# Optimization experiments

Hardware: AMD Instinct MI355X
Metric: run time of the kernel (lower is better)

Reference implementation:

```python
import jax, jax.numpy as jnp
import numpy as np

B, N = 64, 512          # batch (Multiple*BatchSize), nodes per graph
LIT, SEM = 128, 64      # literal / semantic feature widths
ED, HD, OD = 64, 32, 64 # EmbedDim, HalfDim (hardcoded 32), OutputDim
ITERS, ELAYERS = 5, 2   # IteraTimes, EmbedLayer


def setup_inputs() -> dict:
    key = jax.random.key(0)
    ks = jax.random.split(key, 32)
    s = 0.05
    inp = {
        "cfg1": jax.random.randint(ks[0], (B, N, N), 0, 2, dtype=jnp.int32),
        "pfg1": jax.random.randint(ks[1], (B, N, N), 0, 2, dtype=jnp.int32),
        "lit1": jax.random.normal(ks[2], (B, N, LIT), dtype=jnp.float32),
        "sem1": jax.random.normal(ks[3], (B, N, SEM), dtype=jnp.float32),
        "cfg2": jax.random.randint(ks[4], (B, N, N), 0, 2, dtype=jnp.int32),
        "pfg2": jax.random.randint(ks[5], (B, N, N), 0, 2, dtype=jnp.int32),
        "lit2": jax.random.normal(ks[6], (B, N, LIT), dtype=jnp.float32),
        "sem2": jax.random.normal(ks[7], (B, N, SEM), dtype=jnp.float32),
    }
    # branch 1 (MyDataLayer #1) params
    inp["d1w1"] = jax.random.normal(ks[8], (LIT, ED)) * s
    inp["d1b1"] = jnp.zeros((ED,), jnp.float32)
    inp["d2w1"] = jax.random.normal(ks[9], (ED, HD)) * s
    inp["d2b1"] = jnp.zeros((HD,), jnp.float32)
    inp["lk1"] = jax.random.normal(ks[10], (SEM, 4 * HD)) * s
    inp["lrk1"] = jax.random.normal(ks[11], (HD, 4 * HD)) * s
    inp["lb1"] = jnp.zeros((4 * HD,), jnp.float32)
    # branch 2 (MyDataLayer #2) params
    inp["d1w2"] = jax.random.normal(ks[12], (LIT, ED)) * s
    inp["d1b2"] = jnp.zeros((ED,), jnp.float32)
    inp["d2w2"] = jax.random.normal(ks[13], (ED, HD)) * s
    inp["d2b2"] = jnp.zeros((HD,), jnp.float32)
    inp["lk2"] = jax.random.normal(ks[14], (SEM, 4 * HD)) * s
    inp["lrk2"] = jax.random.normal(ks[15], (HD, 4 * HD)) * s
    inp["lb2"] = jnp.zeros((4 * HD,), jnp.float32)
    # shared MyEmbedLayer params
    inp["we_w"] = jax.random.normal(ks[16], (ELAYERS, ED, ED)) * s
    inp["we_b"] = jnp.zeros((ELAYERS, ED), jnp.float32)
    inp["wout"] = jax.random.normal(ks[17], (ED, OD)) * s
    inp["bout"] = jnp.zeros((OD,), jnp.float32)
    return inp


def _lstm(x, k, rk, b):
    # x: [B, T, D]; Keras gate order i, f, c(g), o; sigmoid recurrent activation
    h0 = jnp.zeros((x.shape[0], rk.shape[0]), x.dtype)

    def step(carry, xt):
        h, c = carry
        z = xt @ k + h @ rk + b
        i, f, g, o = jnp.split(z, 4, axis=-1)
        c = jax.nn.sigmoid(f) * c + jax.nn.sigmoid(i) * jnp.tanh(g)
        h = jax.nn.sigmoid(o) * jnp.tanh(c)
        return (h, c), h

    _, hs = jax.lax.scan(step, (h0, h0), jnp.swapaxes(x, 0, 1))
    return jnp.swapaxes(hs, 0, 1)  # [B, T, HD]


def _branch(lit, sem, d1w, d1b, d2w, d2b, lk, lrk, lb):
    mlp = jax.nn.relu(jax.nn.relu(lit @ d1w + d1b) @ d2w + d2b)  # [B,N,HD]
    return jnp.concatenate([mlp, _lstm(sem, lk, lrk, lb)], axis=-1)  # [B,N,ED]


def _embed(inp, adj, we_w, we_b, wout, bout):
    x = jax.nn.relu(inp)
    for _ in range(ITERS):
        t = adj @ x  # [B,N,N] @ [B,N,ED] -> message passing
        for l in range(ELAYERS):
            t = jax.nn.relu(t @ we_w[l] + we_b[l])
        x = jnp.tanh(inp + t)
    return x.sum(axis=1) @ wout + bout  # [B, OD]


def reference(cfg1, pfg1, lit1, sem1, cfg2, pfg2, lit2, sem2,
              d1w1, d1b1, d2w1, d2b1, lk1, lrk1, lb1,
              d1w2, d1b2, d2w2, d2b2, lk2, lrk2, lb2,
              we_w, we_b, wout, bout):
    bb1 = _branch(lit1, sem1, d1w1, d1b1, d2w1, d2b1, lk1, lrk1, lb1)
    e1 = _embed(bb1, cfg1.astype(jnp.float32), we_w, we_b, wout, bout)
    bb2 = _branch(lit2, sem2, d1w2, d1b2, d2w2, d2b2, lk2, lrk2, lb2)
    e2 = _embed(bb2, cfg2.astype(jnp.float32), we_w, we_b, wout, bout)
    num = jnp.sum(e1 * e2, axis=1)
    den = jnp.sqrt(jnp.sum(e1 ** 2, axis=1) * jnp.sum(e2 ** 2, axis=1) + 1e-10)
    return num / den  # [B]
```

## Files before the change

kernel.cpp:

```cpp
#include <hip/hip_runtime.h>

#define DEV static __device__ __forceinline__

typedef float  f32x2 __attribute__((ext_vector_type(2)));
typedef float  f32x4 __attribute__((ext_vector_type(4)));
typedef float  f32x8 __attribute__((ext_vector_type(8)));
typedef __bf16 bf16x8 __attribute__((ext_vector_type(8)));
typedef unsigned short u16x8 __attribute__((ext_vector_type(8)));
typedef int    i32x4 __attribute__((ext_vector_type(4)));

DEV unsigned short f2bf(float f) {
  unsigned u = __builtin_bit_cast(unsigned, f);
  u += 0x7FFFu + ((u >> 16) & 1u);
  return (unsigned short)(u >> 16);
}
DEV float bf2f(unsigned short h) {
  unsigned u = (unsigned)h << 16;
  return __builtin_bit_cast(float, u);
}

DEV f32x4 mfma16(u16x8 a, u16x8 b, f32x4 c) {
  return __builtin_amdgcn_mfma_f32_16x16x32_bf16(
      __builtin_bit_cast(bf16x8, a), __builtin_bit_cast(bf16x8, b), c, 0, 0, 0);
}
DEV i32x4 mfma8(uint4 a, uint4 b, i32x4 c) {
  return __builtin_amdgcn_mfma_i32_16x16x64_i8(
      __builtin_bit_cast(i32x4, a), __builtin_bit_cast(i32x4, b), c, 0, 0, 0);
}

DEV float exp2_hw(float x) { float r; asm("v_exp_f32 %0, %1" : "=v"(r) : "v"(x)); return r; }
DEV float sig_fast(float x) { return __builtin_amdgcn_rcpf(1.f + exp2_hw(-1.44269504f * x)); }
DEV float tanh_fast(float x) { return 1.f - 2.f * __builtin_amdgcn_rcpf(exp2_hw(2.88539008f * x) + 1.f); }

DEV void pkfma(f32x2& acc, f32x2 a, f32x2 b) {
  asm("v_pk_fma_f32 %0, %1, %2, %0" : "+v"(acc) : "v"(a), "v"(b));
}

DEV uint4 expand16(unsigned hw) {
  uint4 r;
  r.x = ((hw         & 0xFu) * 0x00204081u) & 0x01010101u;
  r.y = (((hw >> 4)  & 0xFu) * 0x00204081u) & 0x01010101u;
  r.z = (((hw >> 8)  & 0xFu) * 0x00204081u) & 0x01010101u;
  r.w = (((hw >> 12) & 0xFu) * 0x00204081u) & 0x01010101u;
  return r;
}

DEV void split8(const float* p, u16x8& h, u16x8& l) {
  union { f32x4 q[2]; f32x8 o; } u;
  u.q[0] = *reinterpret_cast<const f32x4*>(p);
  u.q[1] = *reinterpret_cast<const f32x4*>(p + 4);
  #pragma unroll
  for (int i = 0; i < 8; ++i) {
    float v = u.o[i];
    unsigned short hb = f2bf(v);
    h[i] = hb;
    l[i] = f2bf(v - bf2f(hb));
  }
}

template <int K, int NC, int ACT>
__global__ __launch_bounds__(256) void k_ff(
    const float* __restrict__ A1, const float* __restrict__ A2,
    const float* __restrict__ W1, const float* __restrict__ W2,
    const float* __restrict__ b1, const float* __restrict__ b2,
    float* __restrict__ C, int ldC, long brCstride) {
  int bid = blockIdx.x;
  int br = bid >> 8, rbk = bid & 255;
  const float* A = br ? A2 : A1;
  const float* W = br ? W2 : W1;
  const float* bias = br ? b2 : b1;

  __shared__ __attribute__((aligned(16))) unsigned short WTh[NC][K + 8];
  __shared__ __attribute__((aligned(16))) unsigned short WTl[NC][K + 8];
  for (int idx = threadIdx.x; idx < K * NC; idx += 256) {
    int k = idx / NC, c = idx % NC;
    float w = W[idx];
    unsigned short hb = f2bf(w);
    WTh[c][k] = hb;
    WTl[c][k] = f2bf(w - bf2f(hb));
  }
  __syncthreads();

  int wave = threadIdx.x >> 6, lane = threadIdx.x & 63;
  int l15 = lane & 15, g = lane >> 4;
  int row0 = rbk * 128 + wave * 32;

  f32x4 acc[2][NC / 16] = {};
  for (int kk = 0; kk < K; kk += 32) {
    u16x8 ah[2], al[2];
    #pragma unroll
    for (int rt = 0; rt < 2; ++rt)
      split8(A + (size_t)(row0 + rt * 16 + l15) * K + kk + g * 8, ah[rt], al[rt]);
    #pragma unroll
    for (int ct = 0; ct < NC / 16; ++ct) {
      u16x8 wh = *reinterpret_cast<const u16x8*>(&WTh[ct * 16 + l15][kk + g * 8]);
      u16x8 wl = *reinterpret_cast<const u16x8*>(&WTl[ct * 16 + l15][kk + g * 8]);
      #pragma unroll
      for (int rt = 0; rt < 2; ++rt) {
        acc[rt][ct] = mfma16(ah[rt], wh, acc[rt][ct]);
        acc[rt][ct] = mfma16(al[rt], wh, acc[rt][ct]);
        acc[rt][ct] = mfma16(ah[rt], wl, acc[rt][ct]);
      }
    }
  }

  float bv[NC / 16];
  #pragma unroll
  for (int ct = 0; ct < NC / 16; ++ct) bv[ct] = bias[ct * 16 + l15];
  #pragma unroll
  for (int rt = 0; rt < 2; ++rt)
    #pragma unroll
    for (int ct = 0; ct < NC / 16; ++ct)
      #pragma unroll
      for (int r = 0; r < 4; ++r) {
        float v = acc[rt][ct][r] + bv[ct];
        if (ACT) v = fmaxf(v, 0.f);
        C[(size_t)br * brCstride +
          (size_t)(row0 + rt * 16 + g * 4 + r) * ldC + ct * 16 + l15] = v;
      }
}

__global__ __launch_bounds__(256) void k_front(
    const float* __restrict__ xk,
    const float* __restrict__ lrk1, const float* __restrict__ lrk2,
    float* __restrict__ bb,
    const int* __restrict__ cfg1, const int* __restrict__ cfg2,
    unsigned* __restrict__ bits,
    const float* __restrict__ lit1, const float* __restrict__ lit2,
    const float* __restrict__ d1w1, const float* __restrict__ d1w2,
    const float* __restrict__ d1b1, const float* __restrict__ d1b2,
    const float* __restrict__ d2w1, const float* __restrict__ d2w2,
    const float* __restrict__ d2b1, const float* __restrict__ d2b2) {
  __shared__ __attribute__((aligned(16))) unsigned short WT1h[64][136];
  __shared__ __attribute__((aligned(16))) unsigned short WT1l[64][136];
  __shared__ __attribute__((aligned(16))) unsigned short WT2h[32][72];
  __shared__ __attribute__((aligned(16))) unsigned short WT2l[32][72];
  __shared__ __attribute__((aligned(16))) float H1[128][68];
  __shared__ __attribute__((aligned(16))) float sh[4][64];
  __shared__ __attribute__((aligned(16))) float lds_pad[520];

  int bid = blockIdx.x;
  int wave = threadIdx.x >> 6, lane = threadIdx.x & 63;
  if (bid == 0x3FFFFFFF) ((volatile float*)lds_pad)[threadIdx.x & 511] = 1.f;

  if (bid < 32) {
    int gb = bid * 4 + wave;
    int br = gb >> 6, b = gb & 63;
    int u = lane & 31, hi = lane >> 5;
    int c0 = u + (hi << 5), c1 = c0 + 64;
    const float* rkp = br ? lrk2 : lrk1;
    f32x2 rk0p[16], rk1p[16];
    #pragma unroll
    for (int k2 = 0; k2 < 16; ++k2) {
      rk0p[k2] = f32x2{rkp[(2 * k2) * 128 + c0], rkp[(2 * k2 + 1) * 128 + c0]};
      rk1p[k2] = f32x2{rkp[(2 * k2) * 128 + c1], rkp[(2 * k2 + 1) * 128 + c1]};
    }
    float* shw = &sh[wave][0];
    shw[lane] = 0.f;

    const float* xkb = xk + ((size_t)br * 32768 + (size_t)b * 512) * 128;
    float* bbo = bb + ((size_t)br * 32768 + (size_t)b * 512) * 64 + 32;
    float cst = 0.f;

    float z00 = xkb[0 * 128 + c0], z10 = xkb[0 * 128 + c1];
    float z01 = xkb[1 * 128 + c0], z11 = xkb[1 * 128 + c1];
    float z02 = xkb[2 * 128 + c0], z12 = xkb[2 * 128 + c1];
    float z03 = xkb[3 * 128 + c0], z13 = xkb[3 * 128 + c1];
    float z04 = xkb[4 * 128 + c0], z14 = xkb[4 * 128 + c1];
    float z05 = xkb[5 * 128 + c0], z15 = xkb[5 * 128 + c1];
    float z06 = xkb[6 * 128 + c0], z16 = xkb[6 * 128 + c1];
    float z07 = xkb[7 * 128 + c0], z17 = xkb[7 * 128 + c1];

    union Q { f32x4 q; f32x2 p[2]; };

#define LSTM_STEP(T, ZA, ZB) {                                          \
    float a0 = ZA, a1 = ZB;                                             \
    ZA = xkb[((T) + 8) * 128 + c0]; ZB = xkb[((T) + 8) * 128 + c1];     \
    Q q0, q1, q2, q3, q4, q5, q6, q7;                                   \
    q0.q = *reinterpret_cast<const f32x4*>(&shw[32]);                   \
    q1.q = *reinterpret_cast<const f32x4*>(&shw[36]);                   \
    q2.q = *reinterpret_cast<const f32x4*>(&shw[40]);                   \
    q3.q = *reinterpret_cast<const f32x4*>(&shw[44]);                   \
    q4.q = *reinterpret_cast<const f32x4*>(&shw[48]);                   \
    q5.q = *reinterpret_cast<const f32x4*>(&shw[52]);                   \
    q6.q = *reinterpret_cast<const f32x4*>(&shw[56]);                   \
    q7.q = *reinterpret_cast<const f32x4*>(&shw[60]);                   \
    f32x2 A0 = {0.f, 0.f}, A1 = {0.f, 0.f};                             \
    f32x2 B0 = {0.f, 0.f}, B1 = {0.f, 0.f};                             \
    pkfma(A0, q0.p[0], rk0p[0]);  pkfma(B0, q0.p[0], rk1p[0]);          \
    pkfma(A1, q0.p[1], rk0p[1]);  pkfma(B1, q0.p[1], rk1p[1]);          \
    pkfma(A0, q1.p[0], rk0p[2]);  pkfma(B0, q1.p[0], rk1p[2]);          \
    pkfma(A1, q1.p[1], rk0p[3]);  pkfma(B1, q1.p[1], rk1p[3]);          \
    pkfma(A0, q2.p[0], rk0p[4]);  pkfma(B0, q2.p[0], rk1p[4]);          \
    pkfma(A1, q2.p[1], rk0p[5]);  pkfma(B1, q2.p[1], rk1p[5]);          \
    pkfma(A0, q3.p[0], rk0p[6]);  pkfma(B0, q3.p[0], rk1p[6]);          \
    pkfma(A1, q3.p[1], rk0p[7]);  pkfma(B1, q3.p[1], rk1p[7]);          \
    pkfma(A0, q4.p[0], rk0p[8]);  pkfma(B0, q4.p[0], rk1p[8]);          \
    pkfma(A1, q4.p[1], rk0p[9]);  pkfma(B1, q4.p[1], rk1p[9]);          \
    pkfma(A0, q5.p[0], rk0p[10]); pkfma(B0, q5.p[0], rk1p[10]);         \
    pkfma(A1, q5.p[1], rk0p[11]); pkfma(B1, q5.p[1], rk1p[11]);         \
    pkfma(A0, q6.p[0], rk0p[12]); pkfma(B0, q6.p[0], rk1p[12]);         \
    pkfma(A1, q6.p[1], rk0p[13]); pkfma(B1, q6.p[1], rk1p[13]);         \
    pkfma(A0, q7.p[0], rk0p[14]); pkfma(B0, q7.p[0], rk1p[14]);         \
    pkfma(A1, q7.p[1], rk0p[15]); pkfma(B1, q7.p[1], rk1p[15]);         \
    float a0f = a0 + (A0.x + A1.x) + (A0.y + A1.y);                     \
    float a1f = a1 + (B0.x + B1.x) + (B0.y + B1.y);                     \
    float s0 = sig_fast(a0f);                     \
    float s1 = hi ? sig_fast(a1f) : tanh_fast(a1f);  \
    float at = s0 * s1;                           \
    float rc = __shfl_xor(at, 32);                                      \
    cst = s0 * cst + rc;                          \
    float hv = s1 * tanh_fast(cst);                                     \
    shw[lane] = hv;                                                     \
    if (hi) bbo[(T) * 64 + u] = hv;                                     \
  }

    for (int tb = 0; tb < 512; tb += 8) {
      LSTM_STEP(tb + 0, z00, z10)
      LSTM_STEP(tb + 1, z01, z11)
      LSTM_STEP(tb + 2, z02, z12)
      LSTM_STEP(tb + 3, z03, z13)
      LSTM_STEP(tb + 4, z04, z14)
      LSTM_STEP(tb + 5, z05, z15)
      LSTM_STEP(tb + 6, z06, z16)
      LSTM_STEP(tb + 7, z07, z17)
    }
#undef LSTM_STEP
    return;
  }

  if (bid < 288) {
    unsigned worker = (unsigned)(bid - 32) * 256u + threadIdx.x;
    #pragma unroll
    for (int j = 0; j < 16; ++j) {
      unsigned idx = worker + (unsigned)j * 65536u;
      unsigned br2 = idx >> 19;
      unsigned rem = idx & 524287u;
      const int4* p = reinterpret_cast<const int4*>(br2 ? cfg2 : cfg1) + rem * 8;
      unsigned m = 0;
      #pragma unroll
      for (int q = 0; q < 8; ++q) {
        int4 v = p[q];
        unsigned base = q * 4;
        m |= ((unsigned)v.x & 1u) << (base + 0);
        m |= ((unsigned)v.y & 1u) << (base + 1);
        m |= ((unsigned)v.z & 1u) << (base + 2);
        m |= ((unsigned)v.w & 1u) << (base + 3);
      }
      bits[idx] = m;
    }
    return;
  }

  int bid2 = bid - 288;
  int br = bid2 >> 8, rbk = bid2 & 255;
  const float* lit = br ? lit2 : lit1;
  const float* W1  = br ? d1w2 : d1w1;
  const float* B1  = br ? d1b2 : d1b1;
  const float* W2  = br ? d2w2 : d2w1;
  const float* B2  = br ? d2b2 : d2b1;

  for (int idx = threadIdx.x; idx < 8192; idx += 256) {
    int k = idx >> 6, c = idx & 63;
    float w = W1[idx];
    unsigned short hb = f2bf(w);
    WT1h[c][k] = hb;
    WT1l[c][k] = f2bf(w - bf2f(hb));
  }
  for (int idx = threadIdx.x; idx < 2048; idx += 256) {
    int k = idx >> 5, c = idx & 31;
    float w = W2[idx];
    unsigned short hb = f2bf(w);
    WT2h[c][k] = hb;
    WT2l[c][k] = f2bf(w - bf2f(hb));
  }
  __syncthreads();

  int l15 = lane & 15, g = lane >> 4;
  int row0 = rbk * 128 + wave * 32;

  f32x4 acc[2][4] = {};
  #pragma unroll
  for (int kk = 0; kk < 128; kk += 32) {
    u16x8 ah[2], al[2];
    #pragma unroll
    for (int rt = 0; rt < 2; ++rt)
      split8(lit + (size_t)(row0 + rt * 16 + l15) * 128 + kk + g * 8, ah[rt], al[rt]);
    #pragma unroll
    for (int ct = 0; ct < 4; ++ct) {
      u16x8 wh = *reinterpret_cast<const u16x8*>(&WT1h[ct * 16 + l15][kk + g * 8]);
      u16x8 wl = *reinterpret_cast<const u16x8*>(&WT1l[ct * 16 + l15][kk + g * 8]);
      #pragma unroll
      for (int rt = 0; rt < 2; ++rt) {
        acc[rt][ct] = mfma16(ah[rt], wh, acc[rt][ct]);
        acc[rt][ct] = mfma16(al[rt], wh, acc[rt][ct]);
        acc[rt][ct] = mfma16(ah[rt], wl, acc[rt][ct]);
      }
    }
  }
  #pragma unroll
  for (int ct = 0; ct < 4; ++ct) {
    float bv = B1[ct * 16 + l15];
    #pragma unroll
    for (int rt = 0; rt < 2; ++rt)
      #pragma unroll
      for (int r = 0; r < 4; ++r)
        H1[wave * 32 + rt * 16 + g * 4 + r][ct * 16 + l15] =
            fmaxf(acc[rt][ct][r] + bv, 0.f);
  }
  f32x4 acc2[2][2] = {};
  #pragma unroll
  for (int kk = 0; kk < 64; kk += 32) {
    u16x8 ah[2], al[2];
    #pragma unroll
    for (int rt = 0; rt < 2; ++rt)
      split8(&H1[wave * 32 + rt * 16 + l15][kk + g * 8], ah[rt], al[rt]);
    #pragma unroll
    for (int ct = 0; ct < 2; ++ct) {
      u16x8 wh = *reinterpret_cast<const u16x8*>(&WT2h[ct * 16 + l15][kk + g * 8]);
      u16x8 wl = *reinterpret_cast<const u16x8*>(&WT2l[ct * 16 + l15][kk + g * 8]);
      #pragma unroll
      for (int rt = 0; rt < 2; ++rt) {
        acc2[rt][ct] = mfma16(ah[rt], wh, acc2[rt][ct]);
        acc2[rt][ct] = mfma16(al[rt], wh, acc2[rt][ct]);
        acc2[rt][ct] = mfma16(ah[rt], wl, acc2[rt][ct]);
      }
    }
  }
  #pragma unroll
  for (int ct = 0; ct < 2; ++ct) {
    float bv = B2[ct * 16 + l15];
    #pragma unroll
    for (int rt = 0; rt < 2; ++rt)
      #pragma unroll
      for (int r = 0; r < 4; ++r)
        bb[((size_t)br * 32768 + row0 + rt * 16 + g * 4 + r) * 64 + ct * 16 + l15] =
            fmaxf(acc2[rt][ct][r] + bv, 0.f);
  }
}

__global__ __launch_bounds__(256) void k_relu_t(const float* __restrict__ bb,
                                                unsigned short* __restrict__ XTh,
                                                unsigned short* __restrict__ XTl) {
  int bid = blockIdx.x;
  int br = bid >> 9, rem = bid & 511, b = rem >> 3, tile = rem & 7;
  int n0 = tile * 64;
  __shared__ unsigned short xh[64][65], xl[64][65];
  const f32x4* src =
      reinterpret_cast<const f32x4*>(bb + ((size_t)(br * 64 + b) * 512 + n0) * 64);
  #pragma unroll
  for (int i = 0; i < 4; ++i) {
    int f = i * 256 + threadIdx.x;
    f32x4 v = src[f];
    int n = f >> 4, c4 = (f & 15) * 4;
    #pragma unroll
    for (int j = 0; j < 4; ++j) {
      float val = fmaxf(v[j], 0.f);
      unsigned short hb = f2bf(val);
      xh[n][c4 + j] = hb;
      xl[n][c4 + j] = f2bf(val - bf2f(hb));
    }
  }
  __syncthreads();
  int c = threadIdx.x >> 2, j0 = (threadIdx.x & 3) * 16;
  size_t base = ((size_t)(br * 64 + b) * 64 + c) * 512 + n0 + j0;
  u16x8 o0, o1, p0, p1;
  #pragma unroll
  for (int i = 0; i < 8; ++i) {
    o0[i] = xh[j0 + i][c]; o1[i] = xh[j0 + 8 + i][c];
    p0[i] = xl[j0 + i][c]; p1[i] = xl[j0 + 8 + i][c];
  }
  *reinterpret_cast<u16x8*>(XTh + base) = o0;
  *reinterpret_cast<u16x8*>(XTh + base + 8) = o1;
  *reinterpret_cast<u16x8*>(XTl + base) = p0;
  *reinterpret_cast<u16x8*>(XTl + base + 8) = p1;
}

template <int AIN8, int LAST>
__global__ __launch_bounds__(256, 2) void k_iter(
    const unsigned* __restrict__ bits,
    const unsigned short* __restrict__ XTbfh, const unsigned short* __restrict__ XTbfl,
    const char* __restrict__ X8h_in, const char* __restrict__ X8l_in,
    const float* __restrict__ bb,
    const float* __restrict__ we_w, const float* __restrict__ we_b,
    char* __restrict__ X8h_out, char* __restrict__ X8l_out,
    float* __restrict__ Spart) {
  int bid = blockIdx.x;
  int rb = bid >> 7, br = (bid >> 6) & 1, b = bid & 63;
  int n0 = rb * 256;
  __shared__ __attribute__((aligned(16))) unsigned short WT0h[64][72];
  __shared__ __attribute__((aligned(16))) unsigned short WT0l[64][72];
  __shared__ __attribute__((aligned(16))) unsigned short WT1h[64][72];
  __shared__ __attribute__((aligned(16))) unsigned short WT1l[64][72];
  __shared__ __attribute__((aligned(16))) char uni[34816];
  __shared__ float colsum[16][64];
  auto ts  = reinterpret_cast<float(*)[32][68]>(uni);
  auto xh8 = reinterpret_cast<char(*)[65]>(uni);
  auto xl8 = reinterpret_cast<char(*)[65]>(uni + 8320);

  for (int idx = threadIdx.x; idx < 4096; idx += 256) {
    int k = idx >> 6, c = idx & 63;
    float w0 = we_w[k * 64 + c], w1 = we_w[4096 + k * 64 + c];
    unsigned short h0 = f2bf(w0), h1b = f2bf(w1);
    WT0h[c][k] = h0; WT0l[c][k] = f2bf(w0 - bf2f(h0));
    WT1h[c][k] = h1b; WT1l[c][k] = f2bf(w1 - bf2f(h1b));
  }
  __syncthreads();

  int wave = threadIdx.x >> 6, lane = threadIdx.x & 63;
  int l15 = lane & 15, g = lane >> 4;
  int rowbase = n0 + wave * 64;

  union BWU { uint4 v[4]; unsigned w[16]; };
  BWU bw0, bw1, bw2, bw3;
  {
    const unsigned* p0 =
        bits + (size_t)br * 524288 + ((size_t)b * 512 + rowbase + l15) * 16;
    #pragma unroll
    for (int q = 0; q < 4; ++q) {
      bw0.v[q] = reinterpret_cast<const uint4*>(p0)[q];
      bw1.v[q] = reinterpret_cast<const uint4*>(p0 + 256)[q];
      bw2.v[q] = reinterpret_cast<const uint4*>(p0 + 512)[q];
      bw3.v[q] = reinterpret_cast<const uint4*>(p0 + 768)[q];
    }
  }

  float tv[4][4][4];

  if constexpr (!AIN8) {
    size_t xtbase = (size_t)(br * 64 + b) * 64 * 512;
    f32x4 acc[4][4] = {};
    #pragma unroll
    for (int kk = 0; kk < 512; kk += 32) {
      u16x8 a0, a1, a2, a3;
      {
        unsigned w0 = bw0.w[kk >> 5] >> (g * 8), w1 = bw1.w[kk >> 5] >> (g * 8);
        unsigned w2 = bw2.w[kk >> 5] >> (g * 8), w3 = bw3.w[kk >> 5] >> (g * 8);
        union { unsigned u[4]; u16x8 v; } r0, r1, r2, r3;
        #pragma unroll
        for (int i = 0; i < 4; ++i) {
          r0.u[i] = (((w0 >> (2 * i)) & 1u) ? 0x3F80u : 0u) |
                    (((w0 >> (2 * i + 1)) & 1u) ? 0x3F800000u : 0u);
          r1.u[i] = (((w1 >> (2 * i)) & 1u) ? 0x3F80u : 0u) |
                    (((w1 >> (2 * i + 1)) & 1u) ? 0x3F800000u : 0u);
          r2.u[i] = (((w2 >> (2 * i)) & 1u) ? 0x3F80u : 0u) |
                    (((w2 >> (2 * i + 1)) & 1u) ? 0x3F800000u : 0u);
          r3.u[i] = (((w3 >> (2 * i)) & 1u) ? 0x3F80u : 0u) |
                    (((w3 >> (2 * i + 1)) & 1u) ? 0x3F800000u : 0u);
        }
        a0 = r0.v; a1 = r1.v; a2 = r2.v; a3 = r3.v;
      }
      #pragma unroll
      for (int ct = 0; ct < 4; ++ct) {
        size_t off = xtbase + (size_t)(ct * 16 + l15) * 512 + kk + g * 8;
        u16x8 bh = *reinterpret_cast<const u16x8*>(XTbfh + off);
        u16x8 bl = *reinterpret_cast<const u16x8*>(XTbfl + off);
        acc[0][ct] = mfma16(a0, bh, acc[0][ct]);
        acc[0][ct] = mfma16(a0, bl, acc[0][ct]);
        acc[1][ct] = mfma16(a1, bh, acc[1][ct]);
        acc[1][ct] = mfma16(a1, bl, acc[1][ct]);
        acc[2][ct] = mfma16(a2, bh, acc[2][ct]);
        acc[2][ct] = mfma16(a2, bl, acc[2][ct]);
        acc[3][ct] = mfma16(a3, bh, acc[3][ct]);
        acc[3][ct] = mfma16(a3, bl, acc[3][ct]);
      }
    }
    #pragma unroll
    for (int rt = 0; rt < 4; ++rt)
      #pragma unroll
      for (int ct = 0; ct < 4; ++ct)
        #pragma unroll
        for (int r = 0; r < 4; ++r)
          tv[rt][ct][r] = acc[rt][ct][r];
  } else {
    size_t x8base = (size_t)(br * 64 + b) * 64 * 512;
    i32x4 acch[4][4] = {};
    i32x4 accl[4][4] = {};
    #pragma unroll
    for (int c64 = 0; c64 < 8; ++c64) {
      int kk = c64 * 64;
      int wi = (kk >> 5) + (g >> 1), shv = (g & 1) * 16;
      uint4 a0 = expand16((bw0.w[wi] >> shv) & 0xFFFFu);
      uint4 a1 = expand16((bw1.w[wi] >> shv) & 0xFFFFu);
      uint4 a2 = expand16((bw2.w[wi] >> shv) & 0xFFFFu);
      uint4 a3 = expand16((bw3.w[wi] >> shv) & 0xFFFFu);
      #pragma unroll
      for (int ct = 0; ct < 4; ++ct) {
        size_t off = x8base + (size_t)(ct * 16 + l15) * 512 + kk + g * 16;
        uint4 bh = *reinterpret_cast<const uint4*>(X8h_in + off);
        uint4 bl = *reinterpret_cast<const uint4*>(X8l_in + off);
        acch[0][ct] = mfma8(a0, bh, acch[0][ct]);
        accl[0][ct] = mfma8(a0, bl, accl[0][ct]);
        acch[1][ct] = mfma8(a1, bh, acch[1][ct]);
        accl[1][ct] = mfma8(a1, bl, accl[1][ct]);
        acch[2][ct] = mfma8(a2, bh, acch[2][ct]);
        accl[2][ct] = mfma8(a2, bl, accl[2][ct]);
        acch[3][ct] = mfma8(a3, bh, acch[3][ct]);
        accl[3][ct] = mfma8(a3, bl, accl[3][ct]);
      }
    }
    #pragma unroll
    for (int rt = 0; rt < 4; ++rt)
      #pragma unroll
      for (int ct = 0; ct < 4; ++ct)
        #pragma unroll
        for (int r = 0; r < 4; ++r)
          tv[rt][ct][r] = (float)acch[rt][ct][r] * (1.f / 127.f) +
                          (float)accl[rt][ct][r] * (1.f / 16129.f);
  }

  float sacc[4] = {0.f, 0.f, 0.f, 0.f};

  #pragma unroll
  for (int p = 0; p < 2; ++p) {
    if (!LAST && p) __syncthreads();

    #pragma unroll
    for (int rt = 0; rt < 2; ++rt)
      #pragma unroll
      for (int ct = 0; ct < 4; ++ct)
        #pragma unroll
        for (int r = 0; r < 4; ++r)
          ts[wave][rt * 16 + g * 4 + r][ct * 16 + l15] = tv[2 * p + rt][ct][r];

    f32x4 acc1[2][4] = {};
    #pragma unroll
    for (int kk = 0; kk < 64; kk += 32) {
      u16x8 ah[2], al[2];
      #pragma unroll
      for (int rt = 0; rt < 2; ++rt)
        split8(&ts[wave][rt * 16 + l15][kk + g * 8], ah[rt], al[rt]);
      #pragma unroll
      for (int ct = 0; ct < 4; ++ct) {
        u16x8 wh = *reinterpret_cast<const u16x8*>(&WT0h[ct * 16 + l15][kk + g * 8]);
        u16x8 wl = *reinterpret_cast<const u16x8*>(&WT0l[ct * 16 + l15][kk + g * 8]);
        #pragma unroll
        for (int rt = 0; rt < 2; ++rt) {
          acc1[rt][ct] = mfma16(ah[rt], wh, acc1[rt][ct]);
          acc1[rt][ct] = mfma16(al[rt], wh, acc1[rt][ct]);
          acc1[rt][ct] = mfma16(ah[rt], wl, acc1[rt][ct]);
        }
      }
    }
    #pragma unroll
    for (int rt = 0; rt < 2; ++rt)
      #pragma unroll
      for (int ct = 0; ct < 4; ++ct) {
        float bv = we_b[ct * 16 + l15];
        #pragma unroll
        for (int r = 0; r < 4; ++r)
          ts[wave][rt * 16 + g * 4 + r][ct * 16 + l15] =
              fmaxf(acc1[rt][ct][r] + bv, 0.f);
      }

    f32x4 acc2[2][4] = {};
    #pragma unroll
    for (int kk = 0; kk < 64; kk += 32) {
      u16x8 ah[2], al[2];
      #pragma unroll
      for (int rt = 0; rt < 2; ++rt)
        split8(&ts[wave][rt * 16 + l15][kk + g * 8], ah[rt], al[rt]);
      #pragma unroll
      for (int ct = 0; ct < 4; ++ct) {
        u16x8 wh = *reinterpret_cast<const u16x8*>(&WT1h[ct * 16 + l15][kk + g * 8]);
        u16x8 wl = *reinterpret_cast<const u16x8*>(&WT1l[ct * 16 + l15][kk + g * 8]);
        #pragma unroll
        for (int rt = 0; rt < 2; ++rt) {
          acc2[rt][ct] = mfma16(ah[rt], wh, acc2[rt][ct]);
          acc2[rt][ct] = mfma16(al[rt], wh, acc2[rt][ct]);
          acc2[rt][ct] = mfma16(ah[rt], wl, acc2[rt][ct]);
        }
      }
    }

    const float* bbrow =
        bb + ((size_t)(br * 64 + b) * 512 + rowbase + p * 32) * 64;

    if (!LAST) {
      __syncthreads();
      #pragma unroll
      for (int rt = 0; rt < 2; ++rt)
        #pragma unroll
        for (int ct = 0; ct < 4; ++ct) {
          float bv = we_b[64 + ct * 16 + l15];
          #pragma unroll
          for (int r = 0; r < 4; ++r) {
            int rr = rt * 16 + g * 4 + r, cc = ct * 16 + l15;
            float t3 = fmaxf(acc2[rt][ct][r] + bv, 0.f);
            float v = tanh_fast(bbrow[rr * 64 + cc] + t3);
            float s = v * 127.f;
            float qhf = rintf(s);
            float qlf = rintf((s - qhf) * 127.f);
            xh8[wave * 32 + rr][cc] = (char)(int)qhf;
            xl8[wave * 32 + rr][cc] = (char)(int)qlf;
          }
        }
      __syncthreads();
      int c = threadIdx.x >> 2, w4 = threadIdx.x & 3;
      int j0 = w4 * 32;
      size_t base = ((size_t)(br * 64 + b) * 64 + c) * 512 + n0 + w4 * 64 + p * 32;
      union { uint4 v[2]; char bch[32]; } oh, ol;
      #pragma unroll
      for (int i = 0; i < 32; ++i) {
        oh.bch[i] = xh8[j0 + i][c];
        ol.bch[i] = xl8[j0 + i][c];
      }
      *reinterpret_cast<uint4*>(X8h_out + base) = oh.v[0];
      *reinterpret_cast<uint4*>(X8h_out + base + 16) = oh.v[1];
      *reinterpret_cast<uint4*>(X8l_out + base) = ol.v[0];
      *reinterpret_cast<uint4*>(X8l_out + base + 16) = ol.v[1];
    } else {
      #pragma unroll
      for (int ct = 0; ct < 4; ++ct) {
        float bv = we_b[64 + ct * 16 + l15];
        float s = 0.f;
        #pragma unroll
        for (int rt = 0; rt < 2; ++rt)
          #pragma unroll
          for (int r = 0; r < 4; ++r) {
            int rr = rt * 16 + g * 4 + r, cc = ct * 16 + l15;
            float t3 = fmaxf(acc2[rt][ct][r] + bv, 0.f);
            s += tanh_fast(bbrow[rr * 64 + cc] + t3);
          }
        sacc[ct] += s;
      }
    }
  }

  if (LAST) {
    #pragma unroll
    for (int ct = 0; ct < 4; ++ct)
      colsum[wave * 4 + g][ct * 16 + l15] = sacc[ct];
    __syncthreads();
    if (threadIdx.x < 64) {
      float s = 0.f;
      #pragma unroll
      for (int q = 0; q < 16; ++q) s += colsum[q][threadIdx.x];
      Spart[((size_t)(br * 64 + b) * 2 + rb) * 64 + threadIdx.x] = s;
    }
  }
}

__global__ __launch_bounds__(64) void k_final(const float* __restrict__ Spart,
                                              const float* __restrict__ wout,
                                              const float* __restrict__ bout,
                                              float* __restrict__ out) {
  int b = blockIdx.x, c = threadIdx.x;
  __shared__ float s1s[64], s2s[64];
  float s1 = 0.f, s2 = 0.f;
  #pragma unroll
  for (int tl = 0; tl < 2; ++tl) {
    s1 += Spart[((size_t)(0 * 64 + b) * 2 + tl) * 64 + c];
    s2 += Spart[((size_t)(1 * 64 + b) * 2 + tl) * 64 + c];
  }
  s1s[c] = s1; s2s[c] = s2;
  __syncthreads();
  float e1 = bout[c], e2 = bout[c];
  for (int k = 0; k < 64; ++k) {
    float w = wout[k * 64 + c];
    e1 += s1s[k] * w;
    e2 += s2s[k] * w;
  }
  float nm = e1 * e2, dA = e1 * e1, dB = e2 * e2;
  #pragma unroll
  for (int off = 32; off; off >>= 1) {
    nm += __shfl_xor(nm, off);
    dA += __shfl_xor(dA, off);
    dB += __shfl_xor(dB, off);
  }
  if (c == 0) out[b] = nm / sqrtf(dA * dB + 1e-10f);
}

extern "C" void kernel_launch(void* const* d_in, const int* in_sizes, int n_in,
                              void* d_out, int out_size, void* d_ws, size_t ws_size,
                              hipStream_t stream) {
  const int*   cfg1 = (const int*)d_in[0];
  const float* lit1 = (const float*)d_in[2];
  const float* sem1 = (const float*)d_in[3];
  const int*   cfg2 = (const int*)d_in[4];
  const float* lit2 = (const float*)d_in[6];
  const float* sem2 = (const float*)d_in[7];
  const float* d1w1 = (const float*)d_in[8];
  const float* d1b1 = (const float*)d_in[9];
  const float* d2w1 = (const float*)d_in[10];
  const float* d2b1 = (const float*)d_in[11];
  const float* lk1  = (const float*)d_in[12];
  const float* lrk1 = (const float*)d_in[13];
  const float* lb1  = (const float*)d_in[14];
  const float* d1w2 = (const float*)d_in[15];
  const float* d1b2 = (const float*)d_in[16];
  const float* d2w2 = (const float*)d_in[17];
  const float* d2b2 = (const float*)d_in[18];
  const float* lk2  = (const float*)d_in[19];
  const float* lrk2 = (const float*)d_in[20];
  const float* lb2  = (const float*)d_in[21];
  const float* we_w = (const float*)d_in[22];
  const float* we_b = (const float*)d_in[23];
  const float* wout = (const float*)d_in[24];
  const float* bout = (const float*)d_in[25];

  char* ws = (char*)d_ws;
  float* bb   = (float*)ws;
  float* xk   = (float*)(ws + 16777216);
  unsigned short* XTbfh = (unsigned short*)(ws + 16777216);
  unsigned short* XTbfl = (unsigned short*)(ws + 25165824);
  char* A8h = ws + 33554432;
  char* A8l = ws + 37748736;
  char* B8h = ws + 41943040;
  char* B8l = ws + 46137344;
  float* Spart = (float*)(ws + 58720256);
  unsigned* bits = (unsigned*)(ws + 58982400);

  k_ff<64, 128, 0><<<512, 256, 0, stream>>>(sem1, sem2, lk1, lk2, lb1, lb2,
                                            xk, 128, 4194304L);

  k_front<<<800, 256, 0, stream>>>(xk, lrk1, lrk2, bb, cfg1, cfg2, bits,
                                   lit1, lit2, d1w1, d1w2, d1b1, d1b2,
                                   d2w1, d2w2, d2b1, d2b2);

  k_relu_t<<<1024, 256, 0, stream>>>(bb, XTbfh, XTbfl);

  k_iter<0, 0><<<256, 256, 0, stream>>>(bits, XTbfh, XTbfl, nullptr, nullptr,
                                        bb, we_w, we_b, A8h, A8l, Spart);
  k_iter<1, 0><<<256, 256, 0, stream>>>(bits, nullptr, nullptr, A8h, A8l,
                                        bb, we_w, we_b, B8h, B8l, Spart);
  k_iter<1, 0><<<256, 256, 0, stream>>>(bits, nullptr, nullptr, B8h, B8l,
                                        bb, we_w, we_b, A8h, A8l, Spart);
  k_iter<1, 0><<<256, 256, 0, stream>>>(bits, nullptr, nullptr, A8h, A8l,
                                        bb, we_w, we_b, B8h, B8l, Spart);
  k_iter<1, 1><<<256, 256, 0, stream>>>(bits, nullptr, nullptr, B8h, B8l,
                                        bb, we_w, we_b, A8h, A8l, Spart);

  k_final<<<64, 64, 0, stream>>>(Spart, wout, bout, (float*)d_out);
}
```

Before: 308.6 us.

## Remap LSTM recurrence to one lane per hidden unit computing all four gates

The LSTM recurrence previously used a full 64-lane wave per sequence, with each lane computing two gate columns and exchanging results through a cross-half shuffle. Now each 32-lane half-wave handles its own sequence, one from each branch, and each lane computes all four gates for its hidden unit. This halves the LSTM blocks and removes the shuffle from the serial dependency chain. Each lane now does twice the FMAs per step and holds twice the recurrent weights in registers, which lengthens each serial step and may raise register pressure.

```diff
diff --git a/kernel.cpp b/kernel.cpp
--- a/kernel.cpp
+++ b/kernel.cpp
@@ -136,101 +136,90 @@
   __shared__ __attribute__((aligned(16))) unsigned short WT2h[32][72];
   __shared__ __attribute__((aligned(16))) unsigned short WT2l[32][72];
   __shared__ __attribute__((aligned(16))) float H1[128][68];
-  __shared__ __attribute__((aligned(16))) float sh[4][64];
-  __shared__ __attribute__((aligned(16))) float lds_pad[520];
+  __shared__ __attribute__((aligned(16))) float sh[4][2][32];
+  __shared__ __attribute__((aligned(16))) float lds_pad[600];
 
   int bid = blockIdx.x;
   int wave = threadIdx.x >> 6, lane = threadIdx.x & 63;
   if (bid == 0x3FFFFFFF) ((volatile float*)lds_pad)[threadIdx.x & 511] = 1.f;
 
-  if (bid < 32) {
+  if (bid < 16) {
     int gb = bid * 4 + wave;
-    int br = gb >> 6, b = gb & 63;
-    int u = lane & 31, hi = lane >> 5;
-    int c0 = u + (hi << 5), c1 = c0 + 64;
-    const float* rkp = br ? lrk2 : lrk1;
-    f32x2 rk0p[16], rk1p[16];
+    int u = lane & 31, half = lane >> 5;
+    const float* rkp = half ? lrk2 : lrk1;
+    f32x2 rki[16], rkf[16], rkg[16], rko[16];
     #pragma unroll
     for (int k2 = 0; k2 < 16; ++k2) {
-      rk0p[k2] = f32x2{rkp[(2 * k2) * 128 + c0], rkp[(2 * k2 + 1) * 128 + c0]};
-      rk1p[k2] = f32x2{rkp[(2 * k2) * 128 + c1], rkp[(2 * k2 + 1) * 128 + c1]};
-    }
-    float* shw = &sh[wave][0];
-    shw[lane] = 0.f;
-
-    const float* xkb = xk + ((size_t)br * 32768 + (size_t)b * 512) * 128;
-    float* bbo = bb + ((size_t)br * 32768 + (size_t)b * 512) * 64 + 32;
+      const float* r0 = rkp + (2 * k2) * 128;
+      const float* r1 = rkp + (2 * k2 + 1) * 128;
+      rki[k2] = f32x2{r0[u],      r1[u]};
+      rkf[k2] = f32x2{r0[32 + u], r1[32 + u]};
+      rkg[k2] = f32x2{r0[64 + u], r1[64 + u]};
+      rko[k2] = f32x2{r0[96 + u], r1[96 + u]};
+    }
+    float* shw = &sh[wave][half][0];
+    shw[u] = 0.f;
+
+    const float* xkb = xk + ((size_t)half * 32768 + (size_t)gb * 512) * 128;
+    float* bbo = bb + ((size_t)half * 32768 + (size_t)gb * 512) * 64 + 32;
     float cst = 0.f;
 
-    float z00 = xkb[0 * 128 + c0], z10 = xkb[0 * 128 + c1];
-    float z01 = xkb[1 * 128 + c0], z11 = xkb[1 * 128 + c1];
-    float z02 = xkb[2 * 128 + c0], z12 = xkb[2 * 128 + c1];
-    float z03 = xkb[3 * 128 + c0], z13 = xkb[3 * 128 + c1];
-    float z04 = xkb[4 * 128 + c0], z14 = xkb[4 * 128 + c1];
-    float z05 = xkb[5 * 128 + c0], z15 = xkb[5 * 128 + c1];
-    float z06 = xkb[6 * 128 + c0], z16 = xkb[6 * 128 + c1];
-    float z07 = xkb[7 * 128 + c0], z17 = xkb[7 * 128 + c1];
-
-    union Q { f32x4 q; f32x2 p[2]; };
-
-#define LSTM_STEP(T, ZA, ZB) {                                          \
-    float a0 = ZA, a1 = ZB;                                             \
-    ZA = xkb[((T) + 8) * 128 + c0]; ZB = xkb[((T) + 8) * 128 + c1];     \
-    Q q0, q1, q2, q3, q4, q5, q6, q7;                                   \
-    q0.q = *reinterpret_cast<const f32x4*>(&shw[32]);                   \
-    q1.q = *reinterpret_cast<const f32x4*>(&shw[36]);                   \
-    q2.q = *reinterpret_cast<const f32x4*>(&shw[40]);                   \
-    q3.q = *reinterpret_cast<const f32x4*>(&shw[44]);                   \
-    q4.q = *reinterpret_cast<const f32x4*>(&shw[48]);                   \
-    q5.q = *reinterpret_cast<const f32x4*>(&shw[52]);                   \
-    q6.q = *reinterpret_cast<const f32x4*>(&shw[56]);                   \
-    q7.q = *reinterpret_cast<const f32x4*>(&shw[60]);                   \
-    f32x2 A0 = {0.f, 0.f}, A1 = {0.f, 0.f};                             \
-    f32x2 B0 = {0.f, 0.f}, B1 = {0.f, 0.f};                             \
-    pkfma(A0, q0.p[0], rk0p[0]);  pkfma(B0, q0.p[0], rk1p[0]);          \
-    pkfma(A1, q0.p[1], rk0p[1]);  pkfma(B1, q0.p[1], rk1p[1]);          \
-    pkfma(A0, q1.p[0], rk0p[2]);  pkfma(B0, q1.p[0], rk1p[2]);          \
-    pkfma(A1, q1.p[1], rk0p[3]);  pkfma(B1, q1.p[1], rk1p[3]);          \
-    pkfma(A0, q2.p[0], rk0p[4]);  pkfma(B0, q2.p[0], rk1p[4]);          \
-    pkfma(A1, q2.p[1], rk0p[5]);  pkfma(B1, q2.p[1], rk1p[5]);          \
-    pkfma(A0, q3.p[0], rk0p[6]);  pkfma(B0, q3.p[0], rk1p[6]);          \
-    pkfma(A1, q3.p[1], rk0p[7]);  pkfma(B1, q3.p[1], rk1p[7]);          \
-    pkfma(A0, q4.p[0], rk0p[8]);  pkfma(B0, q4.p[0], rk1p[8]);          \
-    pkfma(A1, q4.p[1], rk0p[9]);  pkfma(B1, q4.p[1], rk1p[9]);          \
-    pkfma(A0, q5.p[0], rk0p[10]); pkfma(B0, q5.p[0], rk1p[10]);         \
-    pkfma(A1, q5.p[1], rk0p[11]); pkfma(B1, q5.p[1], rk1p[11]);         \
-    pkfma(A0, q6.p[0], rk0p[12]); pkfma(B0, q6.p[0], rk1p[12]);         \
-    pkfma(A1, q6.p[1], rk0p[13]); pkfma(B1, q6.p[1], rk1p[13]);         \
-    pkfma(A0, q7.p[0], rk0p[14]); pkfma(B0, q7.p[0], rk1p[14]);         \
-    pkfma(A1, q7.p[1], rk0p[15]); pkfma(B1, q7.p[1], rk1p[15]);         \
-    float a0f = a0 + (A0.x + A1.x) + (A0.y + A1.y);                     \
-    float a1f = a1 + (B0.x + B1.x) + (B0.y + B1.y);                     \
-    float s0 = sig_fast(a0f);                     \
-    float s1 = hi ? sig_fast(a1f) : tanh_fast(a1f);  \
-    float at = s0 * s1;                           \
-    float rc = __shfl_xor(at, 32);                                      \
-    cst = s0 * cst + rc;                          \
-    float hv = s1 * tanh_fast(cst);                                     \
-    shw[lane] = hv;                                                     \
-    if (hi) bbo[(T) * 64 + u] = hv;                                     \
-  }
-
-    for (int tb = 0; tb < 512; tb += 8) {
-      LSTM_STEP(tb + 0, z00, z10)
-      LSTM_STEP(tb + 1, z01, z11)
-      LSTM_STEP(tb + 2, z02, z12)
-      LSTM_STEP(tb + 3, z03, z13)
-      LSTM_STEP(tb + 4, z04, z14)
-      LSTM_STEP(tb + 5, z05, z15)
-      LSTM_STEP(tb + 6, z06, z16)
-      LSTM_STEP(tb + 7, z07, z17)
+    float zi0 = xkb[0 * 128 + u], zf0 = xkb[0 * 128 + 32 + u];
+    float zg0 = xkb[0 * 128 + 64 + u], zo0 = xkb[0 * 128 + 96 + u];
+    float zi1 = xkb[1 * 128 + u], zf1 = xkb[1 * 128 + 32 + u];
+    float zg1 = xkb[1 * 128 + 64 + u], zo1 = xkb[1 * 128 + 96 + u];
+    float zi2 = xkb[2 * 128 + u], zf2 = xkb[2 * 128 + 32 + u];
+    float zg2 = xkb[2 * 128 + 64 + u], zo2 = xkb[2 * 128 + 96 + u];
+    float zi3 = xkb[3 * 128 + u], zf3 = xkb[3 * 128 + 32 + u];
+    float zg3 = xkb[3 * 128 + 64 + u], zo3 = xkb[3 * 128 + 96 + u];
+
+    union HQ { f32x4 q; f32x2 p[2]; };
+
+#define LSTM_STEP(T, ZI, ZF, ZG, ZO) {                                  \
+    float ai = ZI, af = ZF, ag = ZG, ao = ZO;                           \
+    ZI = xkb[((T) + 4) * 128 + u];                                      \
+    ZF = xkb[((T) + 4) * 128 + 32 + u];                                 \
+    ZG = xkb[((T) + 4) * 128 + 64 + u];                                 \
+    ZO = xkb[((T) + 4) * 128 + 96 + u];                                 \
+    HQ hq[8];                                                           \
+    _Pragma("unroll")                                                   \
+    for (int j = 0; j < 8; ++j)                                         \
+      hq[j].q = *reinterpret_cast<const f32x4*>(&shw[j * 4]);           \
+    f32x2 AI = {0.f, 0.f}, AF = {0.f, 0.f};                             \
+    f32x2 AG = {0.f, 0.f}, AO = {0.f, 0.f};                             \
+    _Pragma("unroll")                                                   \
+    for (int j = 0; j < 8; ++j) {                                       \
+      pkfma(AI, hq[j].p[0], rki[2 * j]);                                \
+      pkfma(AF, hq[j].p[0], rkf[2 * j]);                                \
+      pkfma(AG, hq[j].p[0], rkg[2 * j]);                                \
+      pkfma(AO, hq[j].p[0], rko[2 * j]);                                \
+      pkfma(AI, hq[j].p[1], rki[2 * j + 1]);                            \
+      pkfma(AF, hq[j].p[1], rkf[2 * j + 1]);                            \
+      pkfma(AG, hq[j].p[1], rkg[2 * j + 1]);                            \
+      pkfma(AO, hq[j].p[1], rko[2 * j + 1]);                            \
+    }                                                                   \
+    ai += AI.x + AI.y; af += AF.x + AF.y;                               \
+    ag += AG.x + AG.y; ao += AO.x + AO.y;                               \
+    float si = sig_fast(ai), sf = sig_fast(af);                         \
+    float tg = tanh_fast(ag), so = sig_fast(ao);                        \
+    cst = sf * cst + si * tg;                                           \
+    float hv = so * tanh_fast(cst);                                     \
+    shw[u] = hv;                                                        \
+    bbo[(T) * 64 + u] = hv;                                             \
+  }
+
+    for (int tb = 0; tb < 512; tb += 4) {
+      LSTM_STEP(tb + 0, zi0, zf0, zg0, zo0)
+      LSTM_STEP(tb + 1, zi1, zf1, zg1, zo1)
+      LSTM_STEP(tb + 2, zi2, zf2, zg2, zo2)
+      LSTM_STEP(tb + 3, zi3, zf3, zg3, zo3)
     }
 #undef LSTM_STEP
     return;
   }
 
-  if (bid < 288) {
-    unsigned worker = (unsigned)(bid - 32) * 256u + threadIdx.x;
+  if (bid < 272) {
+    unsigned worker = (unsigned)(bid - 16) * 256u + threadIdx.x;
     #pragma unroll
     for (int j = 0; j < 16; ++j) {
       unsigned idx = worker + (unsigned)j * 65536u;
@@ -252,7 +241,7 @@
     return;
   }
 
-  int bid2 = bid - 288;
+  int bid2 = bid - 272;
   int br = bid2 >> 8, rbk = bid2 & 255;
   const float* lit = br ? lit2 : lit1;
   const float* W1  = br ? d1w2 : d1w1;
@@ -714,7 +703,7 @@
   k_ff<64, 128, 0><<<512, 256, 0, stream>>>(sem1, sem2, lk1, lk2, lb1, lb2,
                                             xk, 128, 4194304L);
 
-  k_front<<<800, 256, 0, stream>>>(xk, lrk1, lrk2, bb, cfg1, cfg2, bits,
+  k_front<<<784, 256, 0, stream>>>(xk, lrk1, lrk2, bb, cfg1, cfg2, bits,
                                    lit1, lit2, d1w1, d1w2, d1b1, d1b2,
                                    d2w1, d2w2, d2b1, d2b2);
 
```

Result: slower. 327.5 us (+6.1%).
